# Kernel tuning notes

Hardware: AMD Instinct MI355X
Metric: run time of the kernel (lower is better)

Reference implementation:

```python
import jax, jax.numpy as jnp
import numpy as np

C = 256
GROUPS = 32
EPS = 1e-5


def setup_inputs() -> dict:
    key = jax.random.key(0)
    ks = jax.random.split(key, 7)
    B, D, H, W = 2, 8, 48, 48
    x = jax.random.normal(ks[0], (B, C, D, H, W), dtype=jnp.float32)
    norm_w = jnp.ones((C,), jnp.float32)
    norm_b = jnp.zeros((C,), jnp.float32)
    qkv_w = jax.random.normal(ks[1], (3 * C, C), jnp.float32) * (1.0 / np.sqrt(C))
    qkv_b = jnp.zeros((3 * C,), jnp.float32)
    proj_w = jax.random.normal(ks[2], (C, C), jnp.float32) * (1.0 / np.sqrt(C))
    proj_b = jnp.zeros((C,), jnp.float32)
    return {"x": x, "norm_w": norm_w, "norm_b": norm_b,
            "qkv_w": qkv_w, "qkv_b": qkv_b,
            "proj_w": proj_w, "proj_b": proj_b}


def _group_norm(x, w, b):
    B, Cc, D, H, Wd = x.shape
    xg = x.reshape(B, GROUPS, Cc // GROUPS, D, H, Wd)
    mu = xg.mean(axis=(2, 3, 4, 5), keepdims=True)
    var = xg.var(axis=(2, 3, 4, 5), keepdims=True)
    xn = ((xg - mu) * jax.lax.rsqrt(var + EPS)).reshape(B, Cc, D, H, Wd)
    return xn * w[None, :, None, None, None] + b[None, :, None, None, None]


def reference(x, norm_w, norm_b, qkv_w, qkv_b, proj_w, proj_b):
    Cc = x.shape[1]
    h = _group_norm(x, norm_w, norm_b)
    # 1x1x1 conv == channel matmul
    qkv = jnp.einsum('oc,bcdhw->bodhw', qkv_w, h) + qkv_b[None, :, None, None, None]
    q, k, v = jnp.split(qkv, 3, axis=1)
    scale = (Cc // 8) ** (-0.5)
    # [B, D, h, w, H, W] dense spatial attention per depth slice
    attn = jnp.einsum('bcdhw,bcdHW->bdhwHW', q * scale, k)
    # NOTE: original code softmaxes over the LAST axis only (W), not (H,W) jointly.
    attn = jax.nn.softmax(attn, axis=-1)
    out = jnp.einsum('bdhwHW,bcdHW->bcdhw', attn, v)
    out = jnp.einsum('oc,bcdhw->bodhw', proj_w, out) + proj_b[None, :, None, None, None]
    return x + out
```

## Files before the change

kernel.cpp:

```cpp
#include <hip/hip_runtime.h>
#include <hip/hip_bf16.h>

typedef __attribute__((ext_vector_type(8))) short short8;
typedef __attribute__((ext_vector_type(4))) float f32x4;
typedef __attribute__((ext_vector_type(16))) float f32x16;
typedef __attribute__((ext_vector_type(4))) unsigned int u32x4;
typedef unsigned int u32;
typedef unsigned short u16;

#define C_ 256
#define G_ 32
#define ND_ 18432
#define HW_ 2304
#define EPS_ 1e-5f
#define QS2_ 0.25503487f

static __device__ __forceinline__ u16 f2bf(float f) {
  __hip_bfloat16 h = __float2bfloat16(f);
  return __builtin_bit_cast(u16, h);
}

static __device__ __forceinline__ void gll16(const void* g, void* l) {
  __builtin_amdgcn_global_load_lds(
      (const __attribute__((address_space(1))) unsigned int*)g,
      (__attribute__((address_space(3))) unsigned int*)l, 16, 0, 0);
}

__global__ void k_convert_w(const float* __restrict__ qkv_w,
                            const float* __restrict__ proj_w,
                            u16* __restrict__ wout,
                            float* __restrict__ raw) {
  if (blockIdx.x == 0 && threadIdx.x < 128) raw[threadIdx.x] = 0.f;
  int i = blockIdx.x * 256 + threadIdx.x;
  if (i < 196608) wout[i] = f2bf(qkv_w[i]);
  else            wout[i] = f2bf(proj_w[i - 196608]);
}

__global__ __launch_bounds__(256) void k_gn_part(const float* __restrict__ x,
                                                 float* __restrict__ raw) {
  int grp = blockIdx.x >> 2, sub = blockIdx.x & 3;
  const float4* p = (const float4*)(x + (size_t)grp * 147456 + sub * 36864);
  float s1 = 0.f, s2 = 0.f;
  for (int i = threadIdx.x; i < 9216; i += 256) {
    float4 v = p[i];
    s1 += v.x + v.y + v.z + v.w;
    s2 += v.x*v.x + v.y*v.y + v.z*v.z + v.w*v.w;
  }
  for (int off = 1; off < 64; off <<= 1) {
    s1 += __shfl_xor(s1, off, 64);
    s2 += __shfl_xor(s2, off, 64);
  }
  __shared__ float a1[4], a2[4];
  int w = threadIdx.x >> 6;
  if ((threadIdx.x & 63) == 0) { a1[w] = s1; a2[w] = s2; }
  __syncthreads();
  if (threadIdx.x == 0) {
    float t1 = a1[0] + a1[1] + a1[2] + a1[3];
    float t2 = a2[0] + a2[1] + a2[2] + a2[3];
    atomicAdd(&raw[grp * 2], t1);
    atomicAdd(&raw[grp * 2 + 1], t2);
  }
}

__global__ void k_gn_fin(const float* __restrict__ raw, float* __restrict__ stats) {
  int g = threadIdx.x;
  if (g < 64) {
    float mu  = raw[g * 2] / 147456.0f;
    float var = raw[g * 2 + 1] / 147456.0f - mu * mu;
    stats[g * 2]     = mu;
    stats[g * 2 + 1] = rsqrtf(var + EPS_);
  }
}

__global__ __launch_bounds__(256) void k_tnorm(const float* __restrict__ x,
                                               const float* __restrict__ stats,
                                               const float* __restrict__ nw,
                                               const float* __restrict__ nb,
                                               u16* __restrict__ h_t) {
  __shared__ u16 tl[64 * 66];
  int wg = blockIdx.x;
  int nt = wg % 288; int ct = (wg / 288) & 3; int b = wg / 1152;
  int c0 = ct * 64, n0 = nt * 64;
  int tid = threadIdx.x;
#pragma unroll
  for (int p = 0; p < 4; p++) {
    int c_l = p * 16 + (tid >> 4);
    int n4  = (tid & 15) * 4;
    int cg  = c0 + c_l;
    float4 v = *(const float4*)(x + ((size_t)(b * C_ + cg)) * ND_ + n0 + n4);
    float mu = stats[(b * G_ + (cg >> 3)) * 2];
    float rs = stats[(b * G_ + (cg >> 3)) * 2 + 1];
    float w = nw[cg], bia = nb[cg];
    tl[(n4 + 0) * 66 + c_l] = f2bf((v.x - mu) * rs * w + bia);
    tl[(n4 + 1) * 66 + c_l] = f2bf((v.y - mu) * rs * w + bia);
    tl[(n4 + 2) * 66 + c_l] = f2bf((v.z - mu) * rs * w + bia);
    tl[(n4 + 3) * 66 + c_l] = f2bf((v.w - mu) * rs * w + bia);
  }
  __syncthreads();
#pragma unroll
  for (int p = 0; p < 2; p++) {
    int idx = p * 256 + tid;
    int n_l = idx >> 3, c8 = idx & 7;
    const u32* s = (const u32*)((const char*)tl + n_l * 132 + c8 * 16);
    uint4 vv; vv.x = s[0]; vv.y = s[1]; vv.z = s[2]; vv.w = s[3];
    *(uint4*)(h_t + ((size_t)(b * ND_ + n0 + n_l)) * C_ + c0 + c8 * 8) = vv;
  }
}

__global__ __launch_bounds__(256) void k_qk(const u16* __restrict__ h_t,
                                            const u16* __restrict__ w_qkv,
                                            const float* __restrict__ qkv_b,
                                            u16* __restrict__ q_ws,
                                            u16* __restrict__ k_ws) {
  int wg = blockIdx.x;
  int nt = wg % 288; int ot = (wg / 288) & 3; int b = wg / 1152;
  int n0 = nt * 64, o0 = ot * 128;
  int lane = threadIdx.x & 63; int w = threadIdx.x >> 6;
  int g = lane >> 4, lid = lane & 15;
  int n_w = n0 + w * 16;
  f32x4 acc[8];
#pragma unroll
  for (int t = 0; t < 8; t++) acc[t] = (f32x4){0.f, 0.f, 0.f, 0.f};
  const short8* Ab = (const short8*)(h_t + ((size_t)(b * ND_ + n_w + lid)) * C_ + g * 8);
#pragma unroll
  for (int ks = 0; ks < 8; ks++) {
    short8 a = Ab[ks * 4];
#pragma unroll
    for (int t = 0; t < 8; t++) {
      short8 bf = *(const short8*)(w_qkv + ((size_t)(o0 + t * 16 + lid)) * C_ + ks * 32 + g * 8);
      acc[t] = __builtin_amdgcn_mfma_f32_16x16x32_bf16(a, bf, acc[t], 0, 0, 0);
    }
  }
  if (o0 < 256) {
#pragma unroll
    for (int t = 0; t < 8; t++) {
      int o_t = o0 + t * 16;
      float bias = qkv_b[o_t + lid];
#pragma unroll
      for (int r = 0; r < 4; r++) {
        int n_idx = n_w + g * 4 + r;
        q_ws[((size_t)(b * ND_ + n_idx)) * C_ + o_t + lid] = f2bf((acc[t][r] + bias) * QS2_);
      }
    }
  } else {
#pragma unroll
    for (int t = 0; t < 8; t++) {
      int o_t = o0 + t * 16;
      float bias = qkv_b[o_t + lid];
      int oc = o_t - 256 + lid;
#pragma unroll
      for (int r = 0; r < 4; r++) {
        int n_idx = n_w + g * 4 + r;
        int dd = n_idx / 2304, hw = n_idx % 2304;
        int tt = hw / 48, kk = hw % 48;
        size_t off = ((size_t)((b * 8 + dd) * 48 + tt) * 1536 + (oc >> 3) * 48 + kk) * 8 + (oc & 7);
        k_ws[off] = f2bf(acc[t][r] + bias);
      }
    }
  }
}

__global__ __launch_bounds__(256) void k_v(const u16* __restrict__ h_t,
                                           const u16* __restrict__ w_qkv,
                                           const float* __restrict__ qkv_b,
                                           u16* __restrict__ v_ws) {
  int wg = blockIdx.x;
  int nt = wg % 144; int ot = (wg / 144) & 3; int b = wg / 576;
  int n0 = nt * 128, o0 = ot * 64;
  int lane = threadIdx.x & 63; int w = threadIdx.x >> 6;
  int g = lane >> 4, lid = lane & 15;
  int o_w = o0 + w * 16;
  f32x4 acc[8];
#pragma unroll
  for (int t = 0; t < 8; t++) acc[t] = (f32x4){0.f, 0.f, 0.f, 0.f};
  const short8* Ab = (const short8*)(w_qkv + ((size_t)(512 + o_w + lid)) * C_ + g * 8);
#pragma unroll
  for (int ks = 0; ks < 8; ks++) {
    short8 a = Ab[ks * 4];
#pragma unroll
    for (int t = 0; t < 8; t++) {
      short8 bf = *(const short8*)(h_t + ((size_t)(b * ND_ + n0 + t * 16 + lid)) * C_ + ks * 32 + g * 8);
      acc[t] = __builtin_amdgcn_mfma_f32_16x16x32_bf16(a, bf, acc[t], 0, 0, 0);
    }
  }
#pragma unroll
  for (int t = 0; t < 8; t++) {
#pragma unroll
    for (int r = 0; r < 4; r++) {
      int o = o_w + g * 4 + r;
      int n = n0 + t * 16 + lid;
      int d = n / 2304; int hw = n % 2304;
      int grp = hw / 48; int j = hw % 48;
      size_t idx = ((size_t)(((b * 8 + d) * 48 + grp) * 6 + (j >> 3))) * 2048 + o * 8 + (j & 7);
      v_ws[idx] = f2bf(acc[t][r] + qkv_b[512 + o]);
    }
  }
}

__global__ __launch_bounds__(256, 1) void k_attn(const u16* __restrict__ q_ws,
                                                 const u16* __restrict__ k_ws,
                                                 const u16* __restrict__ v_ws,
                                                 u16* __restrict__ ao) {
  __shared__ __align__(16) unsigned char lds[98304];
  int wg = blockIdx.x;
  int virt = (wg & 7) * 36 + (wg >> 3);
  int slice = virt / 18;
  int qt = virt % 18;
  int b = slice >> 3, d = slice & 7;
  int tid = threadIdx.x;
  int lane = tid & 63, w = tid >> 6;
  int l31 = lane & 31, hi = lane >> 5;

  const char* kgb = (const char*)k_ws + (size_t)slice * 1179648;
  const char* vgb = (const char*)v_ws + (size_t)slice * 1179648;

  size_t nbase = (size_t)b * ND_ + d * HW_ + qt * 128 + w * 32;
  const char* qp = (const char*)q_ws + (nbase + l31) * 512 + hi * 16;
  short8 qf[16];
#pragma unroll
  for (int ks = 0; ks < 16; ks++) qf[ks] = *(const short8*)(qp + ks * 32);

  f32x16 acc[8];
#pragma unroll
  for (int i = 0; i < 8; i++) acc[i] = (f32x16)0.0f;

#define STG2(t_, base_) {                                              \
    const char* ks_ = kgb + (size_t)(t_) * 24576 + tid * 16;           \
    const char* vs_ = vgb + (size_t)(t_) * 24576 + tid * 16;           \
    char* kd_ = (char*)lds + (base_) + w * 1024;                       \
    char* vd_ = (char*)lds + (base_) + 24576 + w * 1024;               \
    _Pragma("unroll")                                                  \
    for (int i_ = 0; i_ < 6; i_++) {                                   \
      gll16(ks_ + i_ * 4096, kd_ + i_ * 4096);                         \
      gll16(vs_ + i_ * 4096, vd_ + i_ * 4096);                         \
    } }

  STG2(0, 0);
  __builtin_amdgcn_sched_barrier(0);
  asm volatile("s_waitcnt vmcnt(0)" ::: "memory");
  __builtin_amdgcn_sched_barrier(0);
  __builtin_amdgcn_s_barrier();

  int cur = 0;
  for (int t = 0; t < 48; t++) {
    if (t < 47) STG2(t + 1, (cur ^ 1) * 49152);

    const char* kb = (const char*)lds + cur * 49152;
    const char* vb = kb + 24576;

    f32x16 S0 = (f32x16)0.0f, S1 = (f32x16)0.0f;
#pragma unroll
    for (int ks = 0; ks < 16; ks++) {
      const char* p = kb + (ks * 2 + hi) * 768 + l31 * 16;
      short8 k0 = *(const short8*)(p);
      short8 k1 = *(const short8*)(p + 512);
      S0 = __builtin_amdgcn_mfma_f32_32x32x16_bf16(k0, qf[ks], S0, 0, 0, 0);
      S1 = __builtin_amdgcn_mfma_f32_32x32x16_bf16(k1, qf[ks], S1, 0, 0, 0);
    }

#pragma unroll
    for (int r = 0; r < 16; r++) S0[r] = __builtin_amdgcn_exp2f(S0[r]);
#pragma unroll
    for (int r = 0; r < 8; r++)  S1[r] = __builtin_amdgcn_exp2f(S1[r]);
    float z = 0.f;
#pragma unroll
    for (int r = 0; r < 16; r++) z += S0[r];
#pragma unroll
    for (int r = 0; r < 8; r++)  z += S1[r];
    z += __shfl_xor(z, 32, 64);
    float inv = __builtin_amdgcn_rcpf(z);
#pragma unroll
    for (int r = 0; r < 16; r++) S0[r] *= inv;
#pragma unroll
    for (int r = 0; r < 8; r++)  S1[r] *= inv;

    short8 pa[3];
#pragma unroll
    for (int s = 0; s < 3; s++) {
      const f32x16& P = (s < 2) ? S0 : S1;
      const int a = (s == 1) ? 8 : 0;
      u32 u0, u1, v0, v1;
      asm("v_cvt_pk_bf16_f32 %0, %1, %2" : "=v"(u0) : "v"(P[a + 0]), "v"(P[a + 1]));
      asm("v_cvt_pk_bf16_f32 %0, %1, %2" : "=v"(u1) : "v"(P[a + 2]), "v"(P[a + 3]));
      asm("v_cvt_pk_bf16_f32 %0, %1, %2" : "=v"(v0) : "v"(P[a + 4]), "v"(P[a + 5]));
      asm("v_cvt_pk_bf16_f32 %0, %1, %2" : "=v"(v1) : "v"(P[a + 6]), "v"(P[a + 7]));
      asm("v_permlane32_swap_b32 %0, %1" : "+v"(u0), "+v"(v0));
      asm("v_permlane32_swap_b32 %0, %1" : "+v"(u1), "+v"(v1));
      u32x4 wv; wv[0] = u0; wv[1] = u1; wv[2] = v0; wv[3] = v1;
      pa[s] = __builtin_bit_cast(short8, wv);
    }

#pragma unroll
    for (int s = 0; s < 3; s++) {
      const char* vs = vb + (s * 2 + hi) * 4096 + l31 * 16;
#pragma unroll
      for (int ct = 0; ct < 8; ct++) {
        short8 vf = *(const short8*)(vs + ct * 512);
        acc[ct] = __builtin_amdgcn_mfma_f32_32x32x16_bf16(pa[s], vf, acc[ct], 0, 0, 0);
      }
    }

    __builtin_amdgcn_sched_barrier(0);
    asm volatile("s_waitcnt vmcnt(0)" ::: "memory");
    __builtin_amdgcn_sched_barrier(0);
    __builtin_amdgcn_s_barrier();
    cur ^= 1;
  }

#pragma unroll
  for (int ct = 0; ct < 8; ct++) {
#pragma unroll
    for (int r = 0; r < 16; r++) {
      int ql = (r & 3) + 8 * (r >> 2) + 4 * hi;
      ao[(nbase + ql) * 256 + ct * 32 + l31] = f2bf(acc[ct][r]);
    }
  }
}

__global__ __launch_bounds__(256) void k_proj(const u16* __restrict__ ao,
                                              const u16* __restrict__ w_p,
                                              const float* __restrict__ proj_b,
                                              const float* __restrict__ x,
                                              float* __restrict__ out) {
  int wg = blockIdx.x;
  int nt = wg % 144; int ot = (wg / 144) & 3; int b = wg / 576;
  int n0 = nt * 128, o0 = ot * 64;
  int lane = threadIdx.x & 63; int w = threadIdx.x >> 6;
  int g = lane >> 4, lid = lane & 15;
  int o_w = o0 + w * 16;
  f32x4 acc[8];
#pragma unroll
  for (int t = 0; t < 8; t++) acc[t] = (f32x4){0.f, 0.f, 0.f, 0.f};
  const short8* Ab = (const short8*)(w_p + ((size_t)(o_w + lid)) * C_ + g * 8);
#pragma unroll
  for (int ks = 0; ks < 8; ks++) {
    short8 a = Ab[ks * 4];
#pragma unroll
    for (int t = 0; t < 8; t++) {
      short8 bf = *(const short8*)(ao + ((size_t)(b * ND_ + n0 + t * 16 + lid)) * C_ + ks * 32 + g * 8);
      acc[t] = __builtin_amdgcn_mfma_f32_16x16x32_bf16(a, bf, acc[t], 0, 0, 0);
    }
  }
#pragma unroll
  for (int t = 0; t < 8; t++) {
#pragma unroll
    for (int r = 0; r < 4; r++) {
      int o = o_w + g * 4 + r;
      size_t off = ((size_t)(b * C_ + o)) * ND_ + n0 + t * 16 + lid;
      out[off] = acc[t][r] + proj_b[o] + x[off];
    }
  }
}

extern "C" void kernel_launch(void* const* d_in, const int* in_sizes, int n_in,
                              void* d_out, int out_size, void* d_ws, size_t ws_size,
                              hipStream_t stream) {
  const float* x      = (const float*)d_in[0];
  const float* norm_w = (const float*)d_in[1];
  const float* norm_b = (const float*)d_in[2];
  const float* qkv_w  = (const float*)d_in[3];
  const float* qkv_b  = (const float*)d_in[4];
  const float* proj_w = (const float*)d_in[5];
  const float* proj_b = (const float*)d_in[6];

  char* ws = (char*)d_ws;
  float* stats = (float*)ws;
  float* raw   = (float*)(ws + 512);
  u16* w_qkv = (u16*)(ws + 1024);
  u16* w_p   = (u16*)(ws + 1024 + 393216);
  u16* h_t   = (u16*)(ws + 525312);
  u16* q_ws  = h_t + 9437184;
  u16* k_ws  = q_ws + 9437184;
  u16* v_ws  = k_ws + 9437184;
  u16* ao    = h_t;
  float* out = (float*)d_out;

  if (ws_size < (size_t)525312 + 4ull * 9437184ull * 2ull) return;

  hipLaunchKernelGGL(k_convert_w, dim3(1024), dim3(256), 0, stream, qkv_w, proj_w, w_qkv, raw);
  hipLaunchKernelGGL(k_gn_part,   dim3(256),  dim3(256), 0, stream, x, raw);
  hipLaunchKernelGGL(k_gn_fin,    dim3(1),    dim3(64),  0, stream, raw, stats);
  hipLaunchKernelGGL(k_tnorm,     dim3(2304), dim3(256), 0, stream, x, stats, norm_w, norm_b, h_t);
  hipLaunchKernelGGL(k_qk,        dim3(2304), dim3(256), 0, stream, h_t, w_qkv, qkv_b, q_ws, k_ws);
  hipLaunchKernelGGL(k_v,         dim3(1152), dim3(256), 0, stream, h_t, w_qkv, qkv_b, v_ws);
  hipLaunchKernelGGL(k_attn,      dim3(288),  dim3(256), 0, stream, q_ws, k_ws, v_ws, ao);
  hipLaunchKernelGGL(k_proj,      dim3(1152), dim3(256), 0, stream, ao, w_p, proj_b, x, out);
}
```

Before: 391.3 us.

## Single-buffer V tile in attention to fit two workgroups per CU

The attention kernel's K tile stays double-buffered while the V tile now has a single LDS buffer. This cuts LDS use from 96KB to about 72KB, and launch bounds are raised to 2 blocks per SM so two workgroups can be resident per CU. In exchange, each V load is issued only after the PV matmul of the previous tile and must complete before the next PV step. That adds an extra barrier per iteration and exposes V load latency, which the second resident workgroup is meant to hide. The higher occupancy target may also force register pressure and spills, since each thread holds large accumulator and Q fragment arrays.

```diff
diff --git a/kernel.cpp b/kernel.cpp
--- a/kernel.cpp
+++ b/kernel.cpp
@@ -197,11 +197,11 @@
   }
 }
 
-__global__ __launch_bounds__(256, 1) void k_attn(const u16* __restrict__ q_ws,
+__global__ __launch_bounds__(256, 2) void k_attn(const u16* __restrict__ q_ws,
                                                  const u16* __restrict__ k_ws,
                                                  const u16* __restrict__ v_ws,
                                                  u16* __restrict__ ao) {
-  __shared__ __align__(16) unsigned char lds[98304];
+  __shared__ __align__(16) unsigned char lds[74240];
   int wg = blockIdx.x;
   int virt = (wg & 7) * 36 + (wg >> 3);
   int slice = virt / 18;
@@ -224,29 +224,33 @@
 #pragma unroll
   for (int i = 0; i < 8; i++) acc[i] = (f32x16)0.0f;
 
-#define STG2(t_, base_) {                                              \
-    const char* ks_ = kgb + (size_t)(t_) * 24576 + tid * 16;           \
-    const char* vs_ = vgb + (size_t)(t_) * 24576 + tid * 16;           \
-    char* kd_ = (char*)lds + (base_) + w * 1024;                       \
-    char* vd_ = (char*)lds + (base_) + 24576 + w * 1024;               \
+#define STG_K(t_, base_) {                                             \
+    const char* s_ = kgb + (size_t)(t_) * 24576 + tid * 16;            \
+    char* d_ = (char*)lds + (base_) + w * 1024;                        \
     _Pragma("unroll")                                                  \
-    for (int i_ = 0; i_ < 6; i_++) {                                   \
-      gll16(ks_ + i_ * 4096, kd_ + i_ * 4096);                         \
-      gll16(vs_ + i_ * 4096, vd_ + i_ * 4096);                         \
-    } }
-
-  STG2(0, 0);
+    for (int i_ = 0; i_ < 6; i_++)                                     \
+      gll16(s_ + i_ * 4096, d_ + i_ * 4096);                           \
+  }
+#define STG_V(t_) {                                                    \
+    const char* s_ = vgb + (size_t)(t_) * 24576 + tid * 16;            \
+    char* d_ = (char*)lds + 49152 + w * 1024;                          \
+    _Pragma("unroll")                                                  \
+    for (int i_ = 0; i_ < 6; i_++)                                     \
+      gll16(s_ + i_ * 4096, d_ + i_ * 4096);                           \
+  }
+
+  STG_K(0, 0);
+  STG_V(0);
   __builtin_amdgcn_sched_barrier(0);
   asm volatile("s_waitcnt vmcnt(0)" ::: "memory");
   __builtin_amdgcn_sched_barrier(0);
   __builtin_amdgcn_s_barrier();
 
-  int cur = 0;
+  int kcur = 0;
   for (int t = 0; t < 48; t++) {
-    if (t < 47) STG2(t + 1, (cur ^ 1) * 49152);
-
-    const char* kb = (const char*)lds + cur * 49152;
-    const char* vb = kb + 24576;
+    if (t < 47) STG_K(t + 1, (kcur ^ 1) * 24576);
+
+    const char* kb = (const char*)lds + kcur * 24576;
 
     f32x16 S0 = (f32x16)0.0f, S1 = (f32x16)0.0f;
 #pragma unroll
@@ -290,6 +294,12 @@
       pa[s] = __builtin_bit_cast(short8, wv);
     }
 
+    __builtin_amdgcn_sched_barrier(0);
+    asm volatile("s_waitcnt vmcnt(0)" ::: "memory");
+    __builtin_amdgcn_sched_barrier(0);
+    __builtin_amdgcn_s_barrier();
+
+    const char* vb = (const char*)lds + 49152;
 #pragma unroll
     for (int s = 0; s < 3; s++) {
       const char* vs = vb + (s * 2 + hi) * 4096 + l31 * 16;
@@ -300,11 +310,9 @@
       }
     }
 
-    __builtin_amdgcn_sched_barrier(0);
-    asm volatile("s_waitcnt vmcnt(0)" ::: "memory");
-    __builtin_amdgcn_sched_barrier(0);
     __builtin_amdgcn_s_barrier();
-    cur ^= 1;
+    if (t < 47) STG_V(t + 1);
+    kcur ^= 1;
   }
 
 #pragma unroll
```

Measured after the change: 335.4 us. 14.3% less time.
